# Kernel optimization log

Measured on AMD Instinct MI355X. Metric: run time of the kernel, lower is better.

## Reference

```python
import jax, jax.numpy as jnp
import numpy as np

B, IN, H = 8192, 1024, 2048

def setup_inputs() -> dict:
    key = jax.random.key(0)
    k1, k2, k3, k4, k5 = jax.random.split(key, 5)
    prev_state = jax.random.normal(k1, (B, H), dtype=jnp.float32)
    x = jax.random.normal(k2, (B, IN), dtype=jnp.float32)
    input_weights = jax.random.normal(k3, (H, IN), dtype=jnp.float32) / IN ** 0.5
    input_bias = jnp.zeros((H,), dtype=jnp.float32)
    recurrent_weights = jax.random.normal(k4, (H, H), dtype=jnp.float32) / H ** 0.5
    U_z = jax.random.normal(k5, (H, H), dtype=jnp.float32) / H ** 0.5
    b_u = jnp.zeros((H,), dtype=jnp.float32)
    return {"prev_state": prev_state, "input": x,
            "input_weights": input_weights, "input_bias": input_bias,
            "recurrent_weights": recurrent_weights, "U_z": U_z, "b_u": b_u}

def reference(prev_state, input, input_weights, input_bias, recurrent_weights, U_z, b_u):
    # z = tanh(x @ W_x^T + b_x)
    z = jnp.tanh(input @ input_weights.T + input_bias)
    # u = sigmoid(h @ W_h^T + z @ U_z^T + b_u)
    u = jax.nn.sigmoid(prev_state @ recurrent_weights.T + z @ U_z.T + b_u)
    # convex combination of previous state and candidate
    state = u * prev_state + (1.0 - u) * z
    return state
```

## Files before the change

### kernel.cpp

```cpp
#include <hip/hip_runtime.h>
#include <hip/hip_bf16.h>
#include <cstdint>
#include <cstddef>

#define DEVFN static __device__ __forceinline__

typedef __attribute__((ext_vector_type(8))) short bf16x8;
typedef __attribute__((ext_vector_type(4))) float f32x4;

static constexpr int kB = 8192;
static constexpr int kIN = 1024;
static constexpr int kH = 2048;

DEVFN unsigned short f32_to_bf16(float f) {
  union { float f; unsigned int u; } v; v.f = f;
  unsigned int x = v.u;
  x += 0x7fffu + ((x >> 16) & 1u);
  return (unsigned short)(x >> 16);
}
DEVFN float bf16_to_f32(unsigned short u) {
  union { unsigned int u; float f; } v; v.u = (unsigned int)u << 16;
  return v.f;
}

__global__ void cast_all(const float* __restrict__ x, const float* __restrict__ Wx,
                         const float* __restrict__ Wh, const float* __restrict__ Uz,
                         const float* __restrict__ h,
                         unsigned short* __restrict__ xb, unsigned short* __restrict__ Wxb,
                         unsigned short* __restrict__ Wcat, unsigned short* __restrict__ Acat) {
  const long i = (long)blockIdx.x * blockDim.x + threadIdx.x;
  const float* src; unsigned short* dst; int sh, stride, off; long li;
  if (i < 2097152L)      { li = i;            src = x;  dst = xb;   sh = 8; stride = 1024; off = 0; }
  else if (i < 2621440L) { li = i - 2097152L; src = Wx; dst = Wxb;  sh = 8; stride = 1024; off = 0; }
  else if (i < 3670016L) { li = i - 2621440L; src = Wh; dst = Wcat; sh = 9; stride = 4096; off = 0; }
  else if (i < 4718592L) { li = i - 3670016L; src = Uz; dst = Wcat; sh = 9; stride = 4096; off = 2048; }
  else                   { li = i - 4718592L; src = h;  dst = Acat; sh = 9; stride = 4096; off = 0; }
  float4 v = *(const float4*)(src + li * 4);
  const long row = li >> sh;
  const long col = (li & ((1L << sh) - 1)) * 4;
  unsigned short* d = dst + row * stride + off + col;
  ushort4 o;
  o.x = f32_to_bf16(v.x); o.y = f32_to_bf16(v.y);
  o.z = f32_to_bf16(v.z); o.w = f32_to_bf16(v.w);
  *(ushort4*)d = o;
}

typedef const __attribute__((address_space(1))) unsigned int* gptr_t;
typedef __attribute__((address_space(3))) unsigned int* lptr_t;
DEVFN void gload16(const unsigned short* g, unsigned short* l) {
  __builtin_amdgcn_global_load_lds((gptr_t)g, (lptr_t)l, 16, 0, 0);
}

DEVFN void bar() { __builtin_amdgcn_s_barrier(); }
#define VMC0() asm volatile("s_waitcnt vmcnt(0)" ::: "memory")
#define VMC2() asm volatile("s_waitcnt vmcnt(2)" ::: "memory")


template<int BUF, int QM, int MI0, int MI1>
DEVFN void ldA(bf16x8 (&a)[4][2], const unsigned short* LA0, const unsigned short* LA1) {
#pragma unroll
  for (int mi = MI0; mi < MI1; ++mi) {
    a[mi][0] = *(const bf16x8*)(LA0 + BUF * 16384 + QM * 4096 + mi * 1024);
    a[mi][1] = *(const bf16x8*)(LA1 + BUF * 16384 + QM * 4096 + mi * 1024);
  }
}

template<int BUF, int QN>
DEVFN void ldB(bf16x8 (&b)[4][2], const unsigned short* LB0, const unsigned short* LB1) {
#pragma unroll
  for (int ni = 0; ni < 2; ++ni) {
    const int n = QN * 2 + ni;
    b[n][0] = *(const bf16x8*)(LB0 + BUF * 16384 + n * 1024);
    b[n][1] = *(const bf16x8*)(LB1 + BUF * 16384 + n * 1024);
  }
}

template<int QM, int QN>
DEVFN void mfmaQ(f32x4 (&acc)[8][4], bf16x8 (&a)[4][2], bf16x8 (&b)[4][2]) {
  __builtin_amdgcn_s_setprio(1);
#pragma unroll
  for (int mi = 0; mi < 4; ++mi)
#pragma unroll
    for (int ni = 0; ni < 2; ++ni)
#pragma unroll
      for (int kk = 0; kk < 2; ++kk)
        acc[QM * 4 + mi][QN * 2 + ni] = __builtin_amdgcn_mfma_f32_16x16x32_bf16(
            a[mi][kk], b[QN * 2 + ni][kk], acc[QM * 4 + mi][QN * 2 + ni], 0, 0, 0);
  __builtin_amdgcn_s_setprio(0);
}

template<int EPI>
__global__ __launch_bounds__(512, 1)
void gemm256(const unsigned short* __restrict__ A,
             const unsigned short* __restrict__ W,
             const float* __restrict__ bias,
             int M, int K,
             unsigned short* __restrict__ zOut,
             const unsigned short* __restrict__ hzBuf, int ldhz,
             float* __restrict__ out, int ldo)
{
  __shared__ unsigned short lds[8][8192];
  unsigned short* L = &lds[0][0];

  const int nTM = M >> 8;
  const int bm = blockIdx.x % nTM, bn = blockIdx.x / nTM;
  const int rowBase = bm << 8, colBase = bn << 8;

  const int t = threadIdx.x;
  const int l = t & 63;
  const int w = t >> 6;
  const int lr = l & 15, lg = l >> 4;
  const int wm = w >> 2, wn = w & 3;

  const int kel0 = (lg * 8) ^ ((lr & 7) * 8);
  const unsigned short* LA0 = L + wm * 8192 + lr * 64 + kel0;
  const unsigned short* LA1 = L + wm * 8192 + lr * 64 + (kel0 ^ 32);
  const unsigned short* LB0 = L + 32768 + (wn >> 1) * 8192 + (wn & 1) * 4096 + lr * 64 + kel0;
  const unsigned short* LB1 = L + 32768 + (wn >> 1) * 8192 + (wn & 1) * 4096 + lr * 64 + (kel0 ^ 32);

  const int srow = t >> 3;
  const int scol = (t & 7) * 8;
  const int kcSrc = scol ^ ((srow & 7) * 8);
  const unsigned short* gA = A + (size_t)(rowBase + srow) * K + kcSrc;
  const unsigned short* gB = W + (size_t)(colBase + srow) * K + kcSrc;

#define STAGE(BUF, OP, HALF, KT) do {                                          \
    const unsigned short* gs = ((OP) ? gB : gA)                                \
        + (size_t)((HALF) * 128) * K + (size_t)(KT) * 64;                      \
    unsigned short* ld = L + (OP) * 32768 + ((BUF) * 2 + (HALF)) * 8192        \
        + w * 512;                                                             \
    gload16(gs, ld);                                                           \
    gload16(gs + (size_t)64 * K, ld + 4096);                                   \
  } while (0)

  f32x4 acc[8][4] = {};
  bf16x8 a[4][2], b[4][2];

  STAGE(0, 0, 0, 0); STAGE(0, 0, 1, 0); STAGE(0, 1, 0, 0); STAGE(0, 1, 1, 0);
  STAGE(1, 1, 0, 1); STAGE(1, 1, 1, 1); STAGE(1, 0, 0, 1); STAGE(1, 0, 1, 1);
  VMC0();
  bar();
  ldA<0, 0, 0, 2>(a, LA0, LA1);
  ldB<0, 0>(b, LB0, LB1);

  const int NP = K >> 7;
  for (int j = 0; j < NP; ++j) {
    const bool more = (j + 1 < NP);
    const int ktb1 = 2 * j + 1;
    const int kt0n = more ? 2 * j + 2 : 2 * j;
    const int kt1n = more ? 2 * j + 3 : 2 * j + 1;

    ldA<0, 0, 2, 4>(a, LA0, LA1);
    ldB<0, 1>(b, LB0, LB1);
    STAGE(1, 0, 1, ktb1);
    bar();
    mfmaQ<0, 0>(acc, a, b);
    bar();
    bar();
    mfmaQ<0, 1>(acc, a, b);
    ldA<0, 1, 0, 4>(a, LA0, LA1);
    bar();
    STAGE(0, 1, 0, kt0n);
    bar();
    mfmaQ<1, 0>(acc, a, b);
    VMC2();
    bar();
    ldB<1, 0>(b, LB0, LB1);
    STAGE(0, 1, 1, kt0n);
    bar();
    mfmaQ<1, 1>(acc, a, b);
    ldA<1, 0, 0, 2>(a, LA0, LA1);
    bar();
    ldA<1, 0, 2, 4>(a, LA0, LA1);
    ldB<1, 1>(b, LB0, LB1);
    STAGE(0, 0, 0, kt0n);
    bar();
    mfmaQ<0, 0>(acc, a, b);
    bar();
    STAGE(0, 0, 1, kt0n);
    bar();
    mfmaQ<0, 1>(acc, a, b);
    ldA<1, 1, 0, 4>(a, LA0, LA1);
    bar();
    STAGE(1, 1, 0, kt1n);
    bar();
    mfmaQ<1, 0>(acc, a, b);
    VMC2();
    bar();
    ldB<0, 0>(b, LB0, LB1);
    STAGE(1, 1, 1, kt1n);
    STAGE(1, 0, 0, kt1n);
    bar();
    mfmaQ<1, 1>(acc, a, b);
    ldA<0, 0, 0, 2>(a, LA0, LA1);
    bar();
  }
#undef STAGE

#pragma unroll
  for (int m = 0; m < 8; ++m) {
    const int r0 = rowBase + wm * 128 + m * 16 + lg * 4;
#pragma unroll
    for (int n = 0; n < 4; ++n) {
      const int c = colBase + wn * 64 + n * 16 + lr;
      const float bs = bias[c];
#pragma unroll
      for (int q = 0; q < 4; ++q) {
        const int r = r0 + q;
        const float pre = acc[m][n][q] + bs;
        if (EPI == 0) {
          zOut[(size_t)r * ldhz + c] = f32_to_bf16(tanhf(pre));
        } else {
          const float u = 1.0f / (1.0f + __expf(-pre));
          const float hv = bf16_to_f32(hzBuf[(size_t)r * ldhz + c]);
          const float zv = bf16_to_f32(hzBuf[(size_t)r * ldhz + 2048 + c]);
          out[(size_t)r * ldo + c] = u * hv + (1.0f - u) * zv;
        }
      }
    }
  }
}

extern "C" void kernel_launch(void* const* d_in, const int* in_sizes, int n_in,
                              void* d_out, int out_size, void* d_ws, size_t ws_size,
                              hipStream_t stream) {
  const float* h  = (const float*)d_in[0];
  const float* x  = (const float*)d_in[1];
  const float* Wx = (const float*)d_in[2];
  const float* bx = (const float*)d_in[3];
  const float* Wh = (const float*)d_in[4];
  const float* Uz = (const float*)d_in[5];
  const float* bu = (const float*)d_in[6];
  float* out = (float*)d_out;

  unsigned short* ws   = (unsigned short*)d_ws;
  unsigned short* xb   = ws;
  unsigned short* Wxb  = xb + (size_t)kB * kIN;
  unsigned short* Wcat = Wxb + (size_t)kH * kIN;
  unsigned short* Acat = Wcat + (size_t)kH * 2 * kH;

  cast_all<<<34816, 256, 0, stream>>>(x, Wx, Wh, Uz, h, xb, Wxb, Wcat, Acat);

  const int grid = (kB / 256) * (kH / 256);

  gemm256<0><<<grid, 512, 0, stream>>>(
      xb, Wxb, bx, kB, kIN, Acat + kH, nullptr, 2 * kH, nullptr, 0);

  gemm256<1><<<grid, 512, 0, stream>>>(
      Acat, Wcat, bu, kB, 2 * kH, nullptr, Acat, 2 * kH, out, kH);
}
```

Baseline: 207.2 us.

## Precompute staging pointers, peel last iteration, stage z epilogue through LDS

Global staging addresses move into eight pointers that are bumped by 128 elements each iteration. This replaces the per-iteration size_t multiplies and the conditional tile indices. The final loop iteration is peeled so it no longer issues redundant prefetches of an already-loaded tile. The MFMA loop order changes so the k index is outermost, and the tanh epilogue writes bf16 results to swizzled LDS before issuing coalesced 16-byte global stores instead of scattered 2-byte stores. These changes add code size and one extra barrier, and they reuse LDS after the main loop.

```diff
diff --git a/kernel.cpp b/kernel.cpp
--- a/kernel.cpp
+++ b/kernel.cpp
@@ -79,11 +79,11 @@
 DEVFN void mfmaQ(f32x4 (&acc)[8][4], bf16x8 (&a)[4][2], bf16x8 (&b)[4][2]) {
   __builtin_amdgcn_s_setprio(1);
 #pragma unroll
-  for (int mi = 0; mi < 4; ++mi)
-#pragma unroll
-    for (int ni = 0; ni < 2; ++ni)
-#pragma unroll
-      for (int kk = 0; kk < 2; ++kk)
+  for (int kk = 0; kk < 2; ++kk)
+#pragma unroll
+    for (int mi = 0; mi < 4; ++mi)
+#pragma unroll
+      for (int ni = 0; ni < 2; ++ni)
         acc[QM * 4 + mi][QN * 2 + ni] = __builtin_amdgcn_mfma_f32_16x16x32_bf16(
             a[mi][kk], b[QN * 2 + ni][kk], acc[QM * 4 + mi][QN * 2 + ni], 0, 0, 0);
   __builtin_amdgcn_s_setprio(0);
@@ -121,38 +121,39 @@
   const int srow = t >> 3;
   const int scol = (t & 7) * 8;
   const int kcSrc = scol ^ ((srow & 7) * 8);
-  const unsigned short* gA = A + (size_t)(rowBase + srow) * K + kcSrc;
-  const unsigned short* gB = W + (size_t)(colBase + srow) * K + kcSrc;
-
-#define STAGE(BUF, OP, HALF, KT) do {                                          \
-    const unsigned short* gs = ((OP) ? gB : gA)                                \
-        + (size_t)((HALF) * 128) * K + (size_t)(KT) * 64;                      \
-    unsigned short* ld = L + (OP) * 32768 + ((BUF) * 2 + (HALF)) * 8192        \
-        + w * 512;                                                             \
-    gload16(gs, ld);                                                           \
-    gload16(gs + (size_t)64 * K, ld + 4096);                                   \
+  const unsigned short* pa0 = A + (size_t)(rowBase + srow) * K + kcSrc;
+  const unsigned short* pa1 = pa0 + (size_t)64 * K;
+  const unsigned short* pa2 = pa0 + (size_t)128 * K;
+  const unsigned short* pa3 = pa0 + (size_t)192 * K;
+  const unsigned short* pb0 = W + (size_t)(colBase + srow) * K + kcSrc;
+  const unsigned short* pb1 = pb0 + (size_t)64 * K;
+  const unsigned short* pb2 = pb0 + (size_t)128 * K;
+  const unsigned short* pb3 = pb0 + (size_t)192 * K;
+
+  unsigned short* const sd = L + w * 512;
+#define STAGE(P0, P1, BUF, OP, HALF, OFSE) do {                                \
+    unsigned short* ld = sd + (OP) * 32768 + ((BUF) * 2 + (HALF)) * 8192;      \
+    gload16((P0) + (OFSE), ld);                                                \
+    gload16((P1) + (OFSE), ld + 4096);                                         \
   } while (0)
 
   f32x4 acc[8][4] = {};
   bf16x8 a[4][2], b[4][2];
 
-  STAGE(0, 0, 0, 0); STAGE(0, 0, 1, 0); STAGE(0, 1, 0, 0); STAGE(0, 1, 1, 0);
-  STAGE(1, 1, 0, 1); STAGE(1, 1, 1, 1); STAGE(1, 0, 0, 1); STAGE(1, 0, 1, 1);
+  STAGE(pa0, pa1, 0, 0, 0, 0);  STAGE(pa2, pa3, 0, 0, 1, 0);
+  STAGE(pb0, pb1, 0, 1, 0, 0);  STAGE(pb2, pb3, 0, 1, 1, 0);
+  STAGE(pb0, pb1, 1, 1, 0, 64); STAGE(pb2, pb3, 1, 1, 1, 64);
+  STAGE(pa0, pa1, 1, 0, 0, 64); STAGE(pa2, pa3, 1, 0, 1, 64);
   VMC0();
   bar();
   ldA<0, 0, 0, 2>(a, LA0, LA1);
   ldB<0, 0>(b, LB0, LB1);
 
   const int NP = K >> 7;
-  for (int j = 0; j < NP; ++j) {
-    const bool more = (j + 1 < NP);
-    const int ktb1 = 2 * j + 1;
-    const int kt0n = more ? 2 * j + 2 : 2 * j;
-    const int kt1n = more ? 2 * j + 3 : 2 * j + 1;
-
+  for (int j = 0; j < NP - 1; ++j) {
     ldA<0, 0, 2, 4>(a, LA0, LA1);
     ldB<0, 1>(b, LB0, LB1);
-    STAGE(1, 0, 1, ktb1);
+    STAGE(pa2, pa3, 1, 0, 1, 64);
     bar();
     mfmaQ<0, 0>(acc, a, b);
     bar();
@@ -160,57 +161,120 @@
     mfmaQ<0, 1>(acc, a, b);
     ldA<0, 1, 0, 4>(a, LA0, LA1);
     bar();
-    STAGE(0, 1, 0, kt0n);
+    STAGE(pb0, pb1, 0, 1, 0, 128);
     bar();
     mfmaQ<1, 0>(acc, a, b);
     VMC2();
     bar();
     ldB<1, 0>(b, LB0, LB1);
-    STAGE(0, 1, 1, kt0n);
+    STAGE(pb2, pb3, 0, 1, 1, 128);
     bar();
     mfmaQ<1, 1>(acc, a, b);
     ldA<1, 0, 0, 2>(a, LA0, LA1);
     bar();
     ldA<1, 0, 2, 4>(a, LA0, LA1);
     ldB<1, 1>(b, LB0, LB1);
-    STAGE(0, 0, 0, kt0n);
+    STAGE(pa0, pa1, 0, 0, 0, 128);
     bar();
     mfmaQ<0, 0>(acc, a, b);
     bar();
-    STAGE(0, 0, 1, kt0n);
+    STAGE(pa2, pa3, 0, 0, 1, 128);
     bar();
     mfmaQ<0, 1>(acc, a, b);
     ldA<1, 1, 0, 4>(a, LA0, LA1);
     bar();
-    STAGE(1, 1, 0, kt1n);
+    STAGE(pb0, pb1, 1, 1, 0, 192);
     bar();
     mfmaQ<1, 0>(acc, a, b);
     VMC2();
     bar();
     ldB<0, 0>(b, LB0, LB1);
-    STAGE(1, 1, 1, kt1n);
-    STAGE(1, 0, 0, kt1n);
+    STAGE(pb2, pb3, 1, 1, 1, 192);
+    STAGE(pa0, pa1, 1, 0, 0, 192);
     bar();
     mfmaQ<1, 1>(acc, a, b);
     ldA<0, 0, 0, 2>(a, LA0, LA1);
     bar();
+    pa0 += 128; pa1 += 128; pa2 += 128; pa3 += 128;
+    pb0 += 128; pb1 += 128; pb2 += 128; pb3 += 128;
+  }
+  {
+    ldA<0, 0, 2, 4>(a, LA0, LA1);
+    ldB<0, 1>(b, LB0, LB1);
+    STAGE(pa2, pa3, 1, 0, 1, 64);
+    bar();
+    mfmaQ<0, 0>(acc, a, b);
+    bar();
+    bar();
+    mfmaQ<0, 1>(acc, a, b);
+    ldA<0, 1, 0, 4>(a, LA0, LA1);
+    bar();
+    bar();
+    mfmaQ<1, 0>(acc, a, b);
+    VMC0();
+    bar();
+    ldB<1, 0>(b, LB0, LB1);
+    bar();
+    mfmaQ<1, 1>(acc, a, b);
+    ldA<1, 0, 0, 2>(a, LA0, LA1);
+    bar();
+    ldA<1, 0, 2, 4>(a, LA0, LA1);
+    ldB<1, 1>(b, LB0, LB1);
+    bar();
+    mfmaQ<0, 0>(acc, a, b);
+    bar();
+    bar();
+    mfmaQ<0, 1>(acc, a, b);
+    ldA<1, 1, 0, 4>(a, LA0, LA1);
+    bar();
+    bar();
+    mfmaQ<1, 0>(acc, a, b);
+    bar();
+    bar();
+    mfmaQ<1, 1>(acc, a, b);
+    bar();
   }
 #undef STAGE
 
-#pragma unroll
-  for (int m = 0; m < 8; ++m) {
-    const int r0 = rowBase + wm * 128 + m * 16 + lg * 4;
-#pragma unroll
-    for (int n = 0; n < 4; ++n) {
-      const int c = colBase + wn * 64 + n * 16 + lr;
-      const float bs = bias[c];
-#pragma unroll
-      for (int q = 0; q < 4; ++q) {
-        const int r = r0 + q;
-        const float pre = acc[m][n][q] + bs;
-        if (EPI == 0) {
-          zOut[(size_t)r * ldhz + c] = f32_to_bf16(tanhf(pre));
-        } else {
+  if (EPI == 0) {
+    unsigned short* Z = L;
+#pragma unroll
+    for (int m = 0; m < 8; ++m) {
+      const int rl = wm * 128 + m * 16 + lg * 4;
+#pragma unroll
+      for (int n = 0; n < 4; ++n) {
+        const int cl = wn * 64 + n * 16 + lr;
+        const float bs = bias[colBase + cl];
+#pragma unroll
+        for (int q = 0; q < 4; ++q) {
+          const int r = rl + q;
+          const int sc = cl ^ ((r & 7) * 8);
+          Z[r * 256 + sc] = f32_to_bf16(tanhf(acc[m][n][q] + bs));
+        }
+      }
+    }
+    bar();
+#pragma unroll
+    for (int s = 0; s < 16; ++s) {
+      const int gofs = (s * 512 + t) * 8;
+      const int row = gofs >> 8;
+      const int c0 = gofs & 255;
+      const int sc0 = c0 ^ ((row & 7) * 8);
+      bf16x8 v = *(const bf16x8*)(Z + row * 256 + sc0);
+      *(bf16x8*)(zOut + (size_t)(rowBase + row) * ldhz + colBase + c0) = v;
+    }
+  } else {
+#pragma unroll
+    for (int m = 0; m < 8; ++m) {
+      const int r0 = rowBase + wm * 128 + m * 16 + lg * 4;
+#pragma unroll
+      for (int n = 0; n < 4; ++n) {
+        const int c = colBase + wn * 64 + n * 16 + lr;
+        const float bs = bias[c];
+#pragma unroll
+        for (int q = 0; q < 4; ++q) {
+          const int r = r0 + q;
+          const float pre = acc[m][n][q] + bs;
           const float u = 1.0f / (1.0f + __expf(-pre));
           const float hv = bf16_to_f32(hzBuf[(size_t)r * ldhz + c]);
           const float zv = bf16_to_f32(hzBuf[(size_t)r * ldhz + 2048 + c]);
```

Measured after the change: 211.9 us. 1.02x slower.
